# Optimization experiments

Hardware: AMD Instinct MI355X
Metric: run time of the kernel (lower is better)

The kernel has to match this reference:

```python
import jax, jax.numpy as jnp
import numpy as np
from jax import lax


def setup_inputs() -> dict:
    key = jax.random.key(0)
    ks = jax.random.split(key, 6)
    B, T, F, C = 32, 256, 64, 16
    CO, P, S, K = 16, 64, 32, 4
    x = jax.random.normal(ks[0], (B, T, F, C), dtype=jnp.float32)
    static = jax.random.normal(ks[1], (B, S), dtype=jnp.float32)
    conv_w = jax.random.normal(ks[2], (F, CO, C, K), dtype=jnp.float32) * (1.0 / np.sqrt(C * K))
    conv_b = jax.random.normal(ks[3], (F, CO), dtype=jnp.float32) * 0.01
    W_p = jax.random.normal(ks[4], (F * C + S, P), dtype=jnp.float32) * (1.0 / np.sqrt(F * C + S))
    b_p = jax.random.normal(ks[5], (P,), dtype=jnp.float32) * 0.01
    return {"x": x, "static": static, "conv_w": conv_w, "conv_b": conv_b,
            "W_p": W_p, "b_p": b_p, "dilation": 2}


def _tpc_forward(x, static, conv_w, conv_b, W_p, b_p, dilation):
    B, T, F, C = x.shape
    _, CO, _, K = conv_w.shape
    left_pad = dilation * (K - 1)
    # --- feature-wise causal temporal conv as one grouped dilated conv ---
    # [B, T, F, C] -> [B, F*C, T]  (NCH layout)
    xr = x.transpose(0, 2, 3, 1).reshape(B, F * C, T)
    kr = conv_w.reshape(F * CO, C, K)  # groups = F
    y = lax.conv_general_dilated(
        xr, kr,
        window_strides=(1,),
        padding=[(left_pad, 0)],  # causal left padding
        rhs_dilation=(dilation,),
        dimension_numbers=("NCH", "OIH", "NCH"),
        feature_group_count=F,
    )  # [B, F*CO, T]
    temp_out = y.reshape(B, F, CO, T).transpose(0, 3, 1, 2) + conv_b[None, None, :, :]
    # --- pointwise branch on flattened features + static ---
    flat_x = x.reshape(B, T, F * C)
    static_rep = jnp.broadcast_to(static[:, None, :], (B, T, static.shape[-1]))
    point_in = jnp.concatenate([flat_x, static_rep], axis=-1)  # [B, T, F*C+S]
    point_out = point_in @ W_p + b_p  # [B, T, P]
    point_bcast = jnp.broadcast_to(point_out[:, :, None, :], (B, T, F, point_out.shape[-1]))
    # --- concat fusion + ReLU ---
    fused = jnp.concatenate([x, temp_out, point_bcast], axis=-1)
    return jax.nn.relu(fused)


def reference(x, static, conv_w, conv_b, W_p, b_p, dilation):
    return _tpc_forward(x, static, conv_w, conv_b, W_p, b_p, dilation)
```

## Files before the change

### kernel.cpp

```cpp
#include <hip/hip_runtime.h>

#define B_  32
#define T_  256
#define F_  64
#define C_  16
#define CO_ 16
#define P_  64
#define S_  32
#define K_  4
#define FC_ 1024
#define OUTC 96
#define TT  8
#define NS  14

__global__ __launch_bounds__(512, 4) void tpc_fused(
    const float* __restrict__ x, const float* __restrict__ stat,
    const float* __restrict__ cw, const float* __restrict__ cb,
    const float* __restrict__ Wp, const float* __restrict__ bp,
    float* __restrict__ out)
{
    __shared__ __align__(16) float lds[18944];
    float* xs   = lds;
    float* part = lds + 14336;
    float* pv   = lds + 18432;

    int tid = threadIdx.x;
    int blk = blockIdx.x;
    int b  = blk >> 5;
    int t0 = (blk & 31) * TT;

    #pragma unroll
    for (int it = 0; it < 7; ++it) {
        int v = it * 512 + tid;
        int slice = v >> 8;
        int pos   = v & 255;
        int tg = t0 - 6 + slice;
        float4 val = make_float4(0.f, 0.f, 0.f, 0.f);
        if (tg >= 0)
            val = *(const float4*)(x + ((size_t)(b * T_ + tg)) * FC_ + pos * 4);
        *(float4*)(xs + slice * FC_ + pos * 4) = val;
    }
    __syncthreads();

    {
        int p  = tid & 63;
        int ks = tid >> 6;
        float acc[TT];
        #pragma unroll
        for (int r = 0; r < TT; ++r) acc[r] = 0.f;
        int k0base = ks * 128;
        for (int kk = 0; kk < 128; kk += 4) {
            int k0 = k0base + kk;
            float w0 = Wp[(size_t)(k0 + 0) * P_ + p];
            float w1 = Wp[(size_t)(k0 + 1) * P_ + p];
            float w2 = Wp[(size_t)(k0 + 2) * P_ + p];
            float w3 = Wp[(size_t)(k0 + 3) * P_ + p];
            #pragma unroll
            for (int r = 0; r < TT; ++r) {
                float4 xv = *(const float4*)(xs + (6 + r) * FC_ + k0);
                acc[r] += xv.x * w0 + xv.y * w1 + xv.z * w2 + xv.w * w3;
            }
        }
        #pragma unroll
        for (int r = 0; r < TT; ++r)
            part[(ks * TT + r) * P_ + p] = acc[r];
    }
    __syncthreads();

    int p  = tid & 63;
    int co = tid & 15;
    int fh = tid >> 4;
    int fg = tid >> 6;

    {
        int r = tid >> 6;
        float s = bp[p];
        const float* wst = Wp + (size_t)FC_ * P_;
        #pragma unroll 8
        for (int si = 0; si < S_; ++si)
            s += stat[b * S_ + si] * wst[si * P_ + p];
        #pragma unroll
        for (int ks = 0; ks < 8; ++ks)
            s += part[(ks * TT + r) * P_ + p];
        pv[r * P_ + p] = fmaxf(s, 0.f);
    }

    float cv[2][TT], px[2][TT];
    #pragma unroll
    for (int half = 0; half < 2; ++half) {
        int f = half * 32 + fh;
        float w[64];
        const float4* wg = (const float4*)(cw + ((size_t)(f * CO_ + co)) * (C_ * K_));
        #pragma unroll
        for (int j = 0; j < 16; ++j) {
            float4 t4 = wg[j];
            w[4 * j + 0] = t4.x; w[4 * j + 1] = t4.y;
            w[4 * j + 2] = t4.z; w[4 * j + 3] = t4.w;
        }
        float bias = cb[f * CO_ + co];
        #pragma unroll
        for (int tl = 0; tl < TT; ++tl) {
            float temp = bias;
            #pragma unroll
            for (int k = 0; k < K_; ++k) {
                const float* sp = xs + (tl + 2 * k) * FC_ + f * C_;
                #pragma unroll
                for (int c4 = 0; c4 < 4; ++c4) {
                    float4 xv = *(const float4*)(sp + c4 * 4);
                    temp += xv.x * w[(c4 * 4 + 0) * 4 + k];
                    temp += xv.y * w[(c4 * 4 + 1) * 4 + k];
                    temp += xv.z * w[(c4 * 4 + 2) * 4 + k];
                    temp += xv.w * w[(c4 * 4 + 3) * 4 + k];
                }
            }
            cv[half][tl] = fmaxf(temp, 0.f);
            px[half][tl] = fmaxf(xs[(tl + 6) * FC_ + f * C_ + co], 0.f);
        }
    }
    __syncthreads();

    float pvr[TT];
    #pragma unroll
    for (int tl = 0; tl < TT; ++tl)
        pvr[tl] = pv[tl * P_ + p];

    for (int tl = 0; tl < TT; ++tl) {
        float* st = lds + (tl & 1) * 6144;
        st[fh * OUTC + co]               = px[0][tl];
        st[fh * OUTC + 16 + co]          = cv[0][tl];
        st[(fh + 32) * OUTC + co]        = px[1][tl];
        st[(fh + 32) * OUTC + 16 + co]   = cv[1][tl];
        float pvv = pvr[tl];
        #pragma unroll
        for (int fo = 0; fo < 8; ++fo)
            st[(fo * 8 + fg) * OUTC + 32 + p] = pvv;

        asm volatile("s_waitcnt lgkmcnt(0)" ::: "memory");
        __builtin_amdgcn_sched_barrier(0);
        __builtin_amdgcn_s_barrier();
        __builtin_amdgcn_sched_barrier(0);

        const float4* src = (const float4*)st;
        float4* dst = (float4*)(out + ((size_t)(b * T_ + t0 + tl)) * F_ * OUTC);
        dst[tid]        = src[tid];
        dst[512 + tid]  = src[512 + tid];
        dst[1024 + tid] = src[1024 + tid];
    }
}

extern "C" void kernel_launch(void* const* d_in, const int* in_sizes, int n_in,
                              void* d_out, int out_size, void* d_ws, size_t ws_size,
                              hipStream_t stream) {
    const float* x    = (const float*)d_in[0];
    const float* stat = (const float*)d_in[1];
    const float* cw   = (const float*)d_in[2];
    const float* cb   = (const float*)d_in[3];
    const float* Wp   = (const float*)d_in[4];
    const float* bp   = (const float*)d_in[5];
    float* out = (float*)d_out;

    tpc_fused<<<1024, 512, 0, stream>>>(x, stat, cw, cb, Wp, bp, out);
}
```

Before: 273.7 us.

## Stage all timesteps in LDS once, then stream output per-wave without per-step barriers

Instead of staging one output row per timestep and hitting a block barrier eight times, all eight timesteps of x/conv results are written to LDS (overwriting the x tile) after a single barrier. Each wave then writes one full timestep row, assembling it from the staged x/conv part and the shared pointwise vector so the pointwise values are never replicated in LDS. This cuts barriers and redundant LDS writes, at the cost of an integer divide-by-24 per store for address computation.

```diff
diff --git a/kernel.cpp b/kernel.cpp
--- a/kernel.cpp
+++ b/kernel.cpp
@@ -23,6 +23,7 @@
     float* xs   = lds;
     float* part = lds + 14336;
     float* pv   = lds + 18432;
+    float* st   = lds;
 
     int tid = threadIdx.x;
     int blk = blockIdx.x;
@@ -70,7 +71,6 @@
     int p  = tid & 63;
     int co = tid & 15;
     int fh = tid >> 4;
-    int fg = tid >> 6;
 
     {
         int r = tid >> 6;
@@ -117,34 +117,40 @@
             px[half][tl] = fmaxf(xs[(tl + 6) * FC_ + f * C_ + co], 0.f);
         }
     }
-    __syncthreads();
+    asm volatile("s_waitcnt lgkmcnt(0)" ::: "memory");
+    __builtin_amdgcn_sched_barrier(0);
+    __builtin_amdgcn_s_barrier();
+    __builtin_amdgcn_sched_barrier(0);
 
-    float pvr[TT];
     #pragma unroll
-    for (int tl = 0; tl < TT; ++tl)
-        pvr[tl] = pv[tl * P_ + p];
+    for (int half = 0; half < 2; ++half) {
+        int f = half * 32 + fh;
+        #pragma unroll
+        for (int tl = 0; tl < TT; ++tl) {
+            st[tl * 2048 + f * 32 + co]      = px[half][tl];
+            st[tl * 2048 + f * 32 + 16 + co] = cv[half][tl];
+        }
+    }
+    asm volatile("s_waitcnt lgkmcnt(0)" ::: "memory");
+    __builtin_amdgcn_sched_barrier(0);
+    __builtin_amdgcn_s_barrier();
+    __builtin_amdgcn_sched_barrier(0);
 
-    for (int tl = 0; tl < TT; ++tl) {
-        float* st = lds + (tl & 1) * 6144;
-        st[fh * OUTC + co]               = px[0][tl];
-        st[fh * OUTC + 16 + co]          = cv[0][tl];
-        st[(fh + 32) * OUTC + co]        = px[1][tl];
-        st[(fh + 32) * OUTC + 16 + co]   = cv[1][tl];
-        float pvv = pvr[tl];
+    {
+        int wid  = tid >> 6;
+        int lane = tid & 63;
+        float4* dst = (float4*)(out + ((size_t)(b * T_ + t0 + wid)) * F_ * OUTC);
         #pragma unroll
-        for (int fo = 0; fo < 8; ++fo)
-            st[(fo * 8 + fg) * OUTC + 32 + p] = pvv;
-
-        asm volatile("s_waitcnt lgkmcnt(0)" ::: "memory");
-        __builtin_amdgcn_sched_barrier(0);
-        __builtin_amdgcn_s_barrier();
-        __builtin_amdgcn_sched_barrier(0);
-
-        const float4* src = (const float4*)st;
-        float4* dst = (float4*)(out + ((size_t)(b * T_ + t0 + tl)) * F_ * OUTC);
-        dst[tid]        = src[tid];
-        dst[512 + tid]  = src[512 + tid];
-        dst[1024 + tid] = src[1024 + tid];
+        for (int j = 0; j < 24; ++j) {
+            unsigned q   = j * 64 + lane;
+            unsigned f   = q / 24;
+            unsigned qw4 = q - f * 24;
+            int off = (qw4 < 8)
+                ? (wid * 2048 + (int)(f * 32 + qw4 * 4))
+                : (18432 + wid * 64 + (int)((qw4 - 8) * 4));
+            float4 val = *(const float4*)(lds + off);
+            dst[q] = val;
+        }
     }
 }
 
```

Measured after the change: 280.0 us. 2.3% more time.
